# Kernel tuning notes

Measured on AMD Instinct MI355X. Metric: run time of the kernel, lower is better.

## Reference

```python
import jax, jax.numpy as jnp
import numpy as np

N = 204800  # total nodes in the batched graph
B = 4096    # number of graphs (sessions)
D = 128     # embedding_dim


def setup_inputs() -> dict:
    key = jax.random.key(0)
    ks = jax.random.split(key, 10)
    feat_i = jax.random.normal(ks[0], (N, D), dtype=jnp.float32)
    U_feat = jax.random.normal(ks[1], (B, D), dtype=jnp.float32)
    # per-node click counts >= 1 so log(cnt) is finite
    cnt = jax.random.uniform(ks[2], (N,), dtype=jnp.float32, minval=1.0, maxval=50.0)
    scale = 1.0 / np.sqrt(D)
    W_key = jax.random.normal(ks[3], (D, D), dtype=jnp.float32) * scale
    W_user = jax.random.normal(ks[4], (D, D), dtype=jnp.float32) * scale
    b_user = jax.random.normal(ks[5], (D,), dtype=jnp.float32) * scale
    W_last = jax.random.normal(ks[6], (D, D), dtype=jnp.float32) * scale
    w_e = jax.random.normal(ks[7], (D, 1), dtype=jnp.float32) * scale
    last_nodes = jax.random.randint(ks[8], (B,), 0, N, dtype=jnp.int32)
    segment_ids = jnp.sort(jax.random.randint(ks[9], (N,), 0, B, dtype=jnp.int32))
    return {
        "feat_i": feat_i, "U_feat": U_feat, "cnt": cnt,
        "W_key": W_key, "W_user": W_user, "b_user": b_user,
        "W_last": W_last, "w_e": w_e,
        "last_nodes": last_nodes, "segment_ids": segment_ids,
    }


def reference(feat_i, U_feat, cnt, W_key, W_user, b_user, W_last, w_e,
              last_nodes, segment_ids):
    # linear projections (torch Linear y = x W^T + b; weights here are stored
    # pre-transposed so x @ W is the same math)
    feat_key = feat_i @ W_key                       # [N, D]
    U = U_feat @ W_user + b_user                    # [B, D]
    last_feat = feat_i[last_nodes] @ W_last         # [B, D]
    # dgl.broadcast_nodes: per-graph query replicated onto its nodes
    feat_qry = (U + last_feat)[segment_ids]         # [N, D]
    # additive-sigmoid attention score + log-count bias
    e = jax.nn.sigmoid(feat_qry + feat_key) @ w_e   # [N, 1]
    e = e + jnp.log(cnt)[:, None]                   # [N, 1]
    # segment softmax over ragged per-graph node segments
    m = jax.ops.segment_max(e, segment_ids, num_segments=B)      # [B, 1]
    ex = jnp.exp(e - m[segment_ids])                             # [N, 1]
    s = jax.ops.segment_sum(ex, segment_ids, num_segments=B)     # [B, 1]
    alpha = ex / s[segment_ids]                                  # [N, 1]
    # weighted segment reduce over raw node features (feat_val = feat_i)
    rst = jax.ops.segment_sum(alpha * feat_i, segment_ids, num_segments=B)  # [B, D]
    return rst
```

## Files before the change

### kernel.cpp

```cpp
#include <hip/hip_runtime.h>
#include <hip/hip_bf16.h>
#include <math.h>

#define N_NODES 204800
#define B_GRAPHS 4096
#define DIM 128

typedef __attribute__((ext_vector_type(8))) short bf16x8;
typedef __attribute__((ext_vector_type(4))) float f32x4;

__device__ __forceinline__ float sigf(float x) {
    return 1.0f / (1.0f + __expf(-x));
}

__device__ __forceinline__ unsigned short bfrne(float x) {
    unsigned u = __float_as_uint(x);
    unsigned r = u + 0x7FFFu + ((u >> 16) & 1u);
    return (unsigned short)(r >> 16);
}

__global__ __launch_bounds__(128) void qkernel(
    const float* __restrict__ feat, const float* __restrict__ U_feat,
    const float* __restrict__ W_user, const float* __restrict__ b_user,
    const float* __restrict__ W_last, const int* __restrict__ last_nodes,
    const float* __restrict__ W_key, unsigned short* __restrict__ Wt,
    const int* __restrict__ seg, int* __restrict__ bounds,
    float* __restrict__ q) {
  if (blockIdx.x >= 576) {
    int n = (blockIdx.x - 576) * 128 + threadIdx.x;
    int sc = seg[n];
    int sp = (n == 0) ? -1 : seg[n - 1];
    for (int b = sp + 1; b <= sc; ++b) bounds[b] = (b == 0) ? 0 : n;
    if (n == N_NODES - 1)
      for (int b = sc + 1; b <= B_GRAPHS; ++b) bounds[b] = N_NODES;
    return;
  }
  if (blockIdx.x >= 512) {
    int b = blockIdx.x - 512;
#pragma unroll
    for (int j = 0; j < 2; ++j) {
      int o = b * 256 + j * 128 + threadIdx.x;
      int c = o >> 7, k = o & 127;
      Wt[o] = bfrne(W_key[k * DIM + c]);
    }
    return;
  }
  __shared__ float sU[8][DIM];
  __shared__ float sL[8][DIM];
  const int d = threadIdx.x;
  const int g0 = blockIdx.x * 8;
  for (int g = 0; g < 8; ++g) {
    sU[g][d] = U_feat[(g0 + g) * DIM + d];
    int ln = last_nodes[g0 + g];
    sL[g][d] = feat[ln * DIM + d];
  }
  __syncthreads();
  float acc[8];
#pragma unroll
  for (int g = 0; g < 8; ++g) acc[g] = 0.0f;

  for (int kk = 0; kk < 32; ++kk) {
    float wu[4], wl[4];
#pragma unroll
    for (int j = 0; j < 4; ++j) {
      wu[j] = W_user[(kk * 4 + j) * DIM + d];
      wl[j] = W_last[(kk * 4 + j) * DIM + d];
    }
#pragma unroll
    for (int g = 0; g < 8; ++g) {
      float4 u4 = reinterpret_cast<const float4*>(sU[g])[kk];
      float4 l4 = reinterpret_cast<const float4*>(sL[g])[kk];
      acc[g] += u4.x * wu[0] + u4.y * wu[1] + u4.z * wu[2] + u4.w * wu[3];
      acc[g] += l4.x * wl[0] + l4.y * wl[1] + l4.z * wl[2] + l4.w * wl[3];
    }
  }
  float bu = b_user[d];
  for (int g = 0; g < 8; ++g) q[(g0 + g) * DIM + d] = acc[g] + bu;
}

__global__ __launch_bounds__(512, 4) void ekernel(
    const float* __restrict__ feat, const unsigned short* __restrict__ Wt,
    const float* __restrict__ w_e, const float* __restrict__ cnt,
    const int* __restrict__ seg, const float* __restrict__ q,
    float* __restrict__ e) {
  __shared__ unsigned short sW[128 * DIM];
  __shared__ float sWe[DIM];
  const int tid = threadIdx.x;
  const int base = blockIdx.x * 128;
  const int l = tid & 63, w = tid >> 6;
  const int lr = l & 15, lh = l >> 4;
  const int node = base + w * 16 + lr;

  const int sg = seg[node];
  const float lc = cnt[node];

  const float* rp = feat + (size_t)node * DIM + lh * 8;
  float4 fv[4][2];
#pragma unroll
  for (int ks = 0; ks < 4; ++ks) {
    fv[ks][0] = *reinterpret_cast<const float4*>(rp + ks * 32);
    fv[ks][1] = *reinterpret_cast<const float4*>(rp + ks * 32 + 4);
  }

  const uint4* Wt4 = reinterpret_cast<const uint4*>(Wt);
#pragma unroll
  for (int i = 0; i < 4; ++i) {
    int hw = i * 4096 + tid * 8;
    int row = hw >> 7, k0 = hw & 127;
    uint4 wv = Wt4[i * 512 + tid];
    *reinterpret_cast<uint4*>(&sW[row * DIM + (k0 ^ ((row & 7) << 3))]) = wv;
  }
  if (tid < 32)
    reinterpret_cast<float4*>(sWe)[tid] =
        reinterpret_cast<const float4*>(w_e)[tid];

  const float4* q4p = reinterpret_cast<const float4*>(q);
  float4 qv[4];
#pragma unroll
  for (int c = 0; c < 4; ++c) qv[c] = q4p[(size_t)sg * 32 + c * 4 + lh];

  bf16x8 af[4];
#pragma unroll
  for (int ks = 0; ks < 4; ++ks) {
    union { bf16x8 v; unsigned short u[8]; } a;
    a.u[0] = bfrne(fv[ks][0].x); a.u[1] = bfrne(fv[ks][0].y);
    a.u[2] = bfrne(fv[ks][0].z); a.u[3] = bfrne(fv[ks][0].w);
    a.u[4] = bfrne(fv[ks][1].x); a.u[5] = bfrne(fv[ks][1].y);
    a.u[6] = bfrne(fv[ks][1].z); a.u[7] = bfrne(fv[ks][1].w);
    af[ks] = a.v;
  }

  __syncthreads();

  float4 qv2[4];
#pragma unroll
  for (int c = 0; c < 4; ++c) qv2[c] = q4p[(size_t)sg * 32 + 16 + c * 4 + lh];

  float p = 0.0f;
#pragma unroll
  for (int c = 0; c < 8; ++c) {
    const int row = c * 16 + lr;
    bf16x8 wf[4];
#pragma unroll
    for (int ks = 0; ks < 4; ++ks)
      wf[ks] = *reinterpret_cast<const bf16x8*>(
          &sW[row * DIM + ((ks * 32 + lh * 8) ^ ((row & 7) << 3))]);
    float4 we = *reinterpret_cast<const float4*>(&sWe[c * 16 + lh * 4]);

    f32x4 a0 = f32x4{0.f, 0.f, 0.f, 0.f};
#pragma unroll
    for (int ks = 0; ks < 4; ++ks)
      a0 = __builtin_amdgcn_mfma_f32_16x16x32_bf16(wf[ks], af[ks], a0, 0, 0, 0);

    float4 qc = (c < 4) ? qv[c & 3] : qv2[c & 3];
    p += we.x * sigf(a0[0] + qc.x) + we.y * sigf(a0[1] + qc.y) +
         we.z * sigf(a0[2] + qc.z) + we.w * sigf(a0[3] + qc.w);
  }

  p += __shfl_xor(p, 16, 64);
  p += __shfl_xor(p, 32, 64);
  if (lh == 0) e[node] = p + __logf(lc);
}

__global__ __launch_bounds__(256) void skernel(
    const float* __restrict__ feat, const int* __restrict__ bounds,
    float* __restrict__ e, float* __restrict__ rst) {
  const int b = blockIdx.x;
  const int tid = threadIdx.x;
  const int s0 = bounds[b];
  const int s1 = bounds[b + 1];

  if (s1 <= s0) {
    if (tid < DIM) rst[b * DIM + tid] = 0.0f;
    return;
  }

  __shared__ float red[8];
  __shared__ float part[8 * DIM];
  const int wave = tid >> 6, lane = tid & 63;

  float lm = -3.0e38f;
  for (int i = s0 + tid; i < s1; i += 256) lm = fmaxf(lm, e[i]);
#pragma unroll
  for (int off = 32; off >= 1; off >>= 1) lm = fmaxf(lm, __shfl_xor(lm, off, 64));
  if (lane == 0) red[wave] = lm;
  __syncthreads();
  const float m = fmaxf(fmaxf(red[0], red[1]), fmaxf(red[2], red[3]));

  float ls = 0.0f;
  for (int i = s0 + tid; i < s1; i += 256) {
    float p = __expf(e[i] - m);
    e[i] = p;
    ls += p;
  }
#pragma unroll
  for (int off = 32; off >= 1; off >>= 1) ls += __shfl_xor(ls, off, 64);
  if (lane == 0) red[4 + wave] = ls;
  __syncthreads();
  const float inv = 1.0f / (red[4] + red[5] + red[6] + red[7]);

  const int c = tid & 31;
  const int h = tid >> 5;
  float4 acc = float4{0.f, 0.f, 0.f, 0.f};
  const float4* feat4 = reinterpret_cast<const float4*>(feat);
  for (int n = s0 + h; n < s1; n += 8) {
    float p = e[n];
    float4 f = feat4[n * 32 + c];
    acc.x += p * f.x;
    acc.y += p * f.y;
    acc.z += p * f.z;
    acc.w += p * f.w;
  }
  reinterpret_cast<float4*>(part)[h * 32 + c] = acc;
  __syncthreads();
  if (tid < DIM) {
    float tot = 0.0f;
#pragma unroll
    for (int hh = 0; hh < 8; ++hh) tot += part[hh * DIM + tid];
    rst[b * DIM + tid] = tot * inv;
  }
}

extern "C" void kernel_launch(void* const* d_in, const int* in_sizes, int n_in,
                              void* d_out, int out_size, void* d_ws,
                              size_t ws_size, hipStream_t stream) {
  const float* feat = (const float*)d_in[0];
  const float* U_feat = (const float*)d_in[1];
  const float* cnt = (const float*)d_in[2];
  const float* W_key = (const float*)d_in[3];
  const float* W_user = (const float*)d_in[4];
  const float* b_user = (const float*)d_in[5];
  const float* W_last = (const float*)d_in[6];
  const float* w_e = (const float*)d_in[7];
  const int* last_nodes = (const int*)d_in[8];
  const int* seg = (const int*)d_in[9];
  float* out = (float*)d_out;

  float* q = (float*)d_ws;
  float* e = q + B_GRAPHS * DIM;
  unsigned short* Wt = (unsigned short*)(e + N_NODES);
  int* bounds = (int*)(Wt + DIM * DIM);

  qkernel<<<512 + 64 + N_NODES / 128, 128, 0, stream>>>(
      feat, U_feat, W_user, b_user, W_last, last_nodes, W_key, Wt, seg, bounds, q);
  ekernel<<<N_NODES / 128, 512, 0, stream>>>(feat, Wt, w_e, cnt, seg, q, e);
  skernel<<<B_GRAPHS, 256, 0, stream>>>(feat, bounds, e, out);
}
```

Measured before the change: 63.74 us.

## Use one wave per graph and drop the segment-max pass in softmax reduce

The segment-softmax reduce now assigns one 64-lane wave per graph, four graphs per block, instead of one 256-thread block per graph. Cross-wave shared-memory reductions and barriers go away, replaced by wave shuffles. The max-subtraction pass is removed: exp(e) is taken directly, relying on the scores being bounded (sigmoid-weighted sum plus log count), and it is recomputed in the weighted sum rather than written back to e. This saves a pass over e and the write-back, but it can overflow if scores ever exceed the float exp range, and it does more exp work per node.

```diff
diff --git a/kernel.cpp b/kernel.cpp
--- a/kernel.cpp
+++ b/kernel.cpp
@@ -164,60 +164,45 @@
 
 __global__ __launch_bounds__(256) void skernel(
     const float* __restrict__ feat, const int* __restrict__ bounds,
-    float* __restrict__ e, float* __restrict__ rst) {
-  const int b = blockIdx.x;
-  const int tid = threadIdx.x;
-  const int s0 = bounds[b];
-  const int s1 = bounds[b + 1];
+    const float* __restrict__ e, float* __restrict__ rst) {
+  const int wave = threadIdx.x >> 6;
+  const int lane = threadIdx.x & 63;
+  const int g = blockIdx.x * 4 + wave;
+  const int s0 = bounds[g], s1 = bounds[g + 1];
 
   if (s1 <= s0) {
-    if (tid < DIM) rst[b * DIM + tid] = 0.0f;
+    if (lane < 32)
+      reinterpret_cast<float4*>(rst)[(size_t)g * 32 + lane] =
+          float4{0.f, 0.f, 0.f, 0.f};
     return;
   }
 
-  __shared__ float red[8];
-  __shared__ float part[8 * DIM];
-  const int wave = tid >> 6, lane = tid & 63;
-
-  float lm = -3.0e38f;
-  for (int i = s0 + tid; i < s1; i += 256) lm = fmaxf(lm, e[i]);
-#pragma unroll
-  for (int off = 32; off >= 1; off >>= 1) lm = fmaxf(lm, __shfl_xor(lm, off, 64));
-  if (lane == 0) red[wave] = lm;
-  __syncthreads();
-  const float m = fmaxf(fmaxf(red[0], red[1]), fmaxf(red[2], red[3]));
-
   float ls = 0.0f;
-  for (int i = s0 + tid; i < s1; i += 256) {
-    float p = __expf(e[i] - m);
-    e[i] = p;
-    ls += p;
-  }
+  for (int i = s0 + lane; i < s1; i += 64) ls += __expf(e[i]);
 #pragma unroll
   for (int off = 32; off >= 1; off >>= 1) ls += __shfl_xor(ls, off, 64);
-  if (lane == 0) red[4 + wave] = ls;
-  __syncthreads();
-  const float inv = 1.0f / (red[4] + red[5] + red[6] + red[7]);
-
-  const int c = tid & 31;
-  const int h = tid >> 5;
+  const float inv = 1.0f / ls;
+
+  const int c = lane & 31;
+  const int h = lane >> 5;
   float4 acc = float4{0.f, 0.f, 0.f, 0.f};
   const float4* feat4 = reinterpret_cast<const float4*>(feat);
-  for (int n = s0 + h; n < s1; n += 8) {
-    float p = e[n];
-    float4 f = feat4[n * 32 + c];
-    acc.x += p * f.x;
-    acc.y += p * f.y;
-    acc.z += p * f.z;
-    acc.w += p * f.w;
-  }
-  reinterpret_cast<float4*>(part)[h * 32 + c] = acc;
-  __syncthreads();
-  if (tid < DIM) {
-    float tot = 0.0f;
-#pragma unroll
-    for (int hh = 0; hh < 8; ++hh) tot += part[hh * DIM + tid];
-    rst[b * DIM + tid] = tot * inv;
+  for (int n = s0 + h; n < s1; n += 2) {
+    float pp = __expf(e[n]);
+    float4 f = feat4[(size_t)n * 32 + c];
+    acc.x += pp * f.x;
+    acc.y += pp * f.y;
+    acc.z += pp * f.z;
+    acc.w += pp * f.w;
+  }
+  acc.x += __shfl_xor(acc.x, 32, 64);
+  acc.y += __shfl_xor(acc.y, 32, 64);
+  acc.z += __shfl_xor(acc.z, 32, 64);
+  acc.w += __shfl_xor(acc.w, 32, 64);
+  if (h == 0) {
+    float4 r;
+    r.x = acc.x * inv; r.y = acc.y * inv; r.z = acc.z * inv; r.w = acc.w * inv;
+    reinterpret_cast<float4*>(rst)[(size_t)g * 32 + c] = r;
   }
 }
 
@@ -244,5 +229,5 @@
   qkernel<<<512 + 64 + N_NODES / 128, 128, 0, stream>>>(
       feat, U_feat, W_user, b_user, W_last, last_nodes, W_key, Wt, seg, bounds, q);
   ekernel<<<N_NODES / 128, 512, 0, stream>>>(feat, Wt, w_e, cnt, seg, q, e);
-  skernel<<<B_GRAPHS, 256, 0, stream>>>(feat, bounds, e, out);
-}
+  skernel<<<B_GRAPHS / 4, 256, 0, stream>>>(feat, bounds, e, out);
+}
```

Result: no change. 63.77 us (+0.0%).
